# Kernel tuning notes

Measured on AMD Instinct MI355X. Metric: run time of the kernel, lower is better.

The kernel has to match this reference:

```python
import jax, jax.numpy as jnp
import numpy as np

EPS = 1e-10

def setup_inputs() -> dict:
    key = jax.random.key(0)
    k1, k2, k3 = jax.random.split(key, 3)
    B, R, S, C = 4, 4096, 96, 32
    colors = jax.random.uniform(k1, (B, R, S, C), dtype=jnp.float32)
    densities = jax.random.normal(k2, (B, R, S, 1), dtype=jnp.float32)
    # depths: sorted increasing along the sample axis, in a plausible near/far range
    depths = jnp.sort(jax.random.uniform(k3, (B, R, S, 1), dtype=jnp.float32) * 1.8 + 0.8, axis=2)
    return {"colors": colors, "densities": densities, "depths": depths}

def reference(colors, densities, depths):
    # clamp_mode == 'softplus', white_back == False, foreground-only path
    deltas = depths[:, :, 1:] - depths[:, :, :-1]                      # [B,R,S-1,1]
    colors_mid = (colors[:, :, :-1] + colors[:, :, 1:]) * 0.5          # [B,R,S-1,C]
    densities_mid = (densities[:, :, :-1] + densities[:, :, 1:]) * 0.5
    depths_mid = (depths[:, :, :-1] + depths[:, :, 1:]) * 0.5

    densities_mid = jax.nn.softplus(densities_mid - 1.0)
    density_delta = densities_mid * deltas
    alpha = 1.0 - jnp.exp(-density_delta)                              # [B,R,S-1,1]

    ones = jnp.ones_like(alpha[:, :, :1])
    alpha_shifted = jnp.concatenate([ones, 1.0 - alpha + EPS], axis=-2)  # [B,R,S,1]
    transmittance = jnp.cumprod(alpha_shifted, axis=-2)                # per-ray scan
    weights = alpha * transmittance[:, :, :-1]                         # [B,R,S-1,1]
    weight_bg = transmittance[:, :, -1][..., None]                     # [B,R,1,1]

    composite_rgb = jnp.sum(weights * colors_mid, axis=-2)             # [B,R,C]
    weight_total = jnp.sum(weights, axis=2)                            # [B,R,1]
    composite_depth = jnp.sum(weights * depths_mid, axis=-2) / weight_total
    composite_depth = jnp.where(jnp.isnan(composite_depth), jnp.inf, composite_depth)
    composite_depth = jnp.clip(composite_depth, jnp.min(depths), jnp.max(depths))

    composite_rgb = composite_rgb * 2.0 - 1.0
    return composite_rgb, composite_depth, weights, alpha, weight_bg
```

## Files before the change

kernel.cpp:

```cpp
#include <hip/hip_runtime.h>
#include <math.h>

#define NS 96
#define SM1 95
#define NC 32
#define REPS 1e-10f

__global__ __launch_bounds__(128) void raymarch_scan(
    const float* __restrict__ densities,
    const float* __restrict__ depths,
    float* __restrict__ out_depth,
    float* __restrict__ out_w,
    float* __restrict__ out_alpha,
    float* __restrict__ out_wbg,
    float* __restrict__ ws_coeff,
    float* __restrict__ ws_d0,
    float* __restrict__ ws_d1)
{
    const int ray = blockIdx.x;
    const int t = threadIdx.x;

    __shared__ float s_dep[NS];
    __shared__ float s_den[NS];
    __shared__ float s_alpha[SM1];
    __shared__ float s_scan[SM1];
    __shared__ float s_w[SM1];
    __shared__ float s_a[128];
    __shared__ float s_b[128];

    const float* dep = depths + (size_t)ray * NS;
    const float* den = densities + (size_t)ray * NS;

    if (t < NS) {
        s_dep[t] = dep[t];
        s_den[t] = den[t];
    }
    __syncthreads();

    if (t < SM1) {
        float dm = 0.5f * (s_den[t] + s_den[t + 1]) - 1.0f;
        float sp = fmaxf(dm, 0.0f) + log1pf(expf(-fabsf(dm)));
        float dd = sp * (s_dep[t + 1] - s_dep[t]);
        float a = 1.0f - expf(-dd);
        s_alpha[t] = a;
        s_scan[t] = 1.0f - a + REPS;
        out_alpha[(size_t)ray * SM1 + t] = a;
    }
    __syncthreads();

    #pragma unroll
    for (int off = 1; off < SM1; off <<= 1) {
        float x = 1.0f;
        if (t >= off && t < SM1) x = s_scan[t - off];
        __syncthreads();
        if (t >= off && t < SM1) s_scan[t] *= x;
        __syncthreads();
    }

    float w = 0.0f;
    if (t < SM1) {
        float T = (t == 0) ? 1.0f : s_scan[t - 1];
        w = s_alpha[t] * T;
        s_w[t] = w;
        out_w[(size_t)ray * SM1 + t] = w;
    }
    s_a[t] = w;
    s_b[t] = (t < SM1) ? w * 0.5f * (s_dep[t] + s_dep[t + 1]) : 0.0f;
    __syncthreads();

    #pragma unroll
    for (int off = 64; off > 0; off >>= 1) {
        if (t < off) {
            s_a[t] += s_a[t + off];
            s_b[t] += s_b[t + off];
        }
        __syncthreads();
    }

    if (t == 0) {
        out_wbg[ray] = s_scan[SM1 - 1];
        float cd = s_b[0] / s_a[0];
        if (cd != cd) cd = __builtin_inff();
        out_depth[ray] = cd;
        ws_d0[ray] = s_dep[0];
        ws_d1[ray] = s_dep[NS - 1];
    }
    if (t < NS) {
        float wprev = (t >= 1)  ? s_w[t - 1] : 0.0f;
        float wcur  = (t < SM1) ? s_w[t]     : 0.0f;
        ws_coeff[(size_t)ray * NS + t] = 0.5f * (wprev + wcur);
    }
}

__global__ __launch_bounds__(256) void raymarch_color(
    const float* __restrict__ colors,
    const float* __restrict__ ws_coeff,
    float* __restrict__ out_rgb)
{
    const int ray = blockIdx.x;
    const int t = threadIdx.x;

    __shared__ float s_coeff[NS];
    __shared__ float s_red[256 * 4];

    const float4* col4 = (const float4*)(colors + (size_t)ray * NS * NC);
    float4 v0 = col4[t];
    float4 v1 = col4[256 + t];
    float4 v2 = col4[512 + t];

    if (t < NS) s_coeff[t] = ws_coeff[(size_t)ray * NS + t];
    __syncthreads();

    float c0 = s_coeff[t >> 3];
    float c1 = s_coeff[(256 + t) >> 3];
    float c2 = s_coeff[(512 + t) >> 3];
    float4 acc;
    acc.x = fmaf(c0, v0.x, fmaf(c1, v1.x, c2 * v2.x));
    acc.y = fmaf(c0, v0.y, fmaf(c1, v1.y, c2 * v2.y));
    acc.z = fmaf(c0, v0.z, fmaf(c1, v1.z, c2 * v2.z));
    acc.w = fmaf(c0, v0.w, fmaf(c1, v1.w, c2 * v2.w));

    s_red[t * 4 + 0] = acc.x;
    s_red[t * 4 + 1] = acc.y;
    s_red[t * 4 + 2] = acc.z;
    s_red[t * 4 + 3] = acc.w;
    __syncthreads();

    if (t < NC) {
        float sum = 0.0f;
        #pragma unroll
        for (int m = 0; m < 32; ++m) {
            sum += s_red[m * 32 + t];
        }
        out_rgb[(size_t)ray * NC + t] = 2.0f * sum - 1.0f;
    }
}

__global__ __launch_bounds__(256) void raymarch_finalize(
    const float* __restrict__ ws_d0,
    const float* __restrict__ ws_d1,
    float* __restrict__ out_depth,
    int rays)
{
    __shared__ float s_mn[256];
    __shared__ float s_mx[256];
    const int tid = threadIdx.x;

    float mn = __builtin_inff();
    float mx = -__builtin_inff();
    for (int r = tid; r < rays; r += 256) {
        mn = fminf(mn, ws_d0[r]);
        mx = fmaxf(mx, ws_d1[r]);
    }
    s_mn[tid] = mn;
    s_mx[tid] = mx;
    __syncthreads();
    for (int off = 128; off > 0; off >>= 1) {
        if (tid < off) {
            s_mn[tid] = fminf(s_mn[tid], s_mn[tid + off]);
            s_mx[tid] = fmaxf(s_mx[tid], s_mx[tid + off]);
        }
        __syncthreads();
    }
    const float dmin = s_mn[0];
    const float dmax = s_mx[0];

    const int r = blockIdx.x * 256 + tid;
    if (r < rays) {
        float cd = out_depth[r];
        cd = fminf(fmaxf(cd, dmin), dmax);
        out_depth[r] = cd;
    }
}

extern "C" void kernel_launch(void* const* d_in, const int* in_sizes, int n_in,
                              void* d_out, int out_size, void* d_ws, size_t ws_size,
                              hipStream_t stream) {
    const float* colors    = (const float*)d_in[0];
    const float* densities = (const float*)d_in[1];
    const float* depths    = (const float*)d_in[2];

    const int rays = in_sizes[2] / NS;

    float* out = (float*)d_out;
    float* out_rgb   = out;
    float* out_depth = out_rgb + (size_t)rays * NC;
    float* out_w     = out_depth + rays;
    float* out_alpha = out_w + (size_t)rays * SM1;
    float* out_wbg   = out_alpha + (size_t)rays * SM1;

    float* ws       = (float*)d_ws;
    float* ws_d0    = ws;
    float* ws_d1    = ws + rays;
    float* ws_coeff = ws + 2 * (size_t)rays;

    raymarch_scan<<<rays, 128, 0, stream>>>(
        densities, depths,
        out_depth, out_w, out_alpha, out_wbg, ws_coeff, ws_d0, ws_d1);

    raymarch_color<<<rays, 256, 0, stream>>>(colors, ws_coeff, out_rgb);

    raymarch_finalize<<<(rays + 255) / 256, 256, 0, stream>>>(
        ws_d0, ws_d1, out_depth, rays);
}
```

Baseline: 314.7 us.

## Use wavefront-per-ray shuffle scan and multi-ray blocks for color reduction

The scan kernel now maps one 64-lane wavefront to each ray, four rays per block. Each lane handles two samples, and the prefix product and reductions use warp shuffles, which removes shared memory and the many __syncthreads barriers. The color kernel now processes 16 rays per block, with each thread accumulating 48 samples in registers and one xor-shuffle combining the two halves. This replaces the per-ray shared-memory reduction and launches fewer blocks. Fast __expf/__logf intrinsics replace expf/log1pf, which risks small accuracy differences in softplus and alpha. The code also assumes the ray count is divisible by 16.

```diff
diff --git a/kernel.cpp b/kernel.cpp
--- a/kernel.cpp
+++ b/kernel.cpp
@@ -6,7 +6,7 @@
 #define NC 32
 #define REPS 1e-10f
 
-__global__ __launch_bounds__(128) void raymarch_scan(
+__global__ __launch_bounds__(256) void raymarch_scan(
     const float* __restrict__ densities,
     const float* __restrict__ depths,
     float* __restrict__ out_depth,
@@ -17,78 +17,100 @@
     float* __restrict__ ws_d0,
     float* __restrict__ ws_d1)
 {
-    const int ray = blockIdx.x;
-    const int t = threadIdx.x;
-
-    __shared__ float s_dep[NS];
-    __shared__ float s_den[NS];
-    __shared__ float s_alpha[SM1];
-    __shared__ float s_scan[SM1];
-    __shared__ float s_w[SM1];
-    __shared__ float s_a[128];
-    __shared__ float s_b[128];
+    const int ray  = blockIdx.x * 4 + (threadIdx.x >> 6);
+    const int lane = threadIdx.x & 63;
 
     const float* dep = depths + (size_t)ray * NS;
     const float* den = densities + (size_t)ray * NS;
 
-    if (t < NS) {
-        s_dep[t] = dep[t];
-        s_den[t] = den[t];
-    }
-    __syncthreads();
-
-    if (t < SM1) {
-        float dm = 0.5f * (s_den[t] + s_den[t + 1]) - 1.0f;
-        float sp = fmaxf(dm, 0.0f) + log1pf(expf(-fabsf(dm)));
-        float dd = sp * (s_dep[t + 1] - s_dep[t]);
-        float a = 1.0f - expf(-dd);
-        s_alpha[t] = a;
-        s_scan[t] = 1.0f - a + REPS;
-        out_alpha[(size_t)ray * SM1 + t] = a;
-    }
-    __syncthreads();
-
-    #pragma unroll
-    for (int off = 1; off < SM1; off <<= 1) {
-        float x = 1.0f;
-        if (t >= off && t < SM1) x = s_scan[t - off];
-        __syncthreads();
-        if (t >= off && t < SM1) s_scan[t] *= x;
-        __syncthreads();
-    }
-
-    float w = 0.0f;
-    if (t < SM1) {
-        float T = (t == 0) ? 1.0f : s_scan[t - 1];
-        w = s_alpha[t] * T;
-        s_w[t] = w;
-        out_w[(size_t)ray * SM1 + t] = w;
-    }
-    s_a[t] = w;
-    s_b[t] = (t < SM1) ? w * 0.5f * (s_dep[t] + s_dep[t + 1]) : 0.0f;
-    __syncthreads();
-
-    #pragma unroll
-    for (int off = 64; off > 0; off >>= 1) {
-        if (t < off) {
-            s_a[t] += s_a[t + off];
-            s_b[t] += s_b[t + off];
-        }
-        __syncthreads();
-    }
-
-    if (t == 0) {
-        out_wbg[ray] = s_scan[SM1 - 1];
-        float cd = s_b[0] / s_a[0];
+    const int i1 = 64 + lane;
+    float dep0 = dep[lane];
+    float den0 = den[lane];
+    float dep1 = (i1 < NS) ? dep[i1] : 0.0f;
+    float den1 = (i1 < NS) ? den[i1] : 0.0f;
+
+    float dn0 = __shfl(dep0, (lane + 1) & 63);
+    float en0 = __shfl(den0, (lane + 1) & 63);
+    float d64 = __shfl(dep1, 0);
+    float e64 = __shfl(den1, 0);
+    if (lane == 63) { dn0 = d64; en0 = e64; }
+    float dn1 = __shfl(dep1, (lane + 1) & 63);
+    float en1 = __shfl(den1, (lane + 1) & 63);
+
+    float dm0  = 0.5f * (den0 + en0) - 1.0f;
+    float sp0  = fmaxf(dm0, 0.0f) + __logf(1.0f + __expf(-fabsf(dm0)));
+    float a0   = 1.0f - __expf(-sp0 * (dn0 - dep0));
+    float mid0 = 0.5f * (dep0 + dn0);
+
+    float a1 = 0.0f, mid1 = 0.0f;
+    if (lane < 31) {
+        float dm1 = 0.5f * (den1 + en1) - 1.0f;
+        float sp1 = fmaxf(dm1, 0.0f) + __logf(1.0f + __expf(-fabsf(dm1)));
+        a1   = 1.0f - __expf(-sp1 * (dn1 - dep1));
+        mid1 = 0.5f * (dep1 + dn1);
+    }
+
+    float oma0 = 1.0f - a0 + REPS;
+    float oma1 = (lane < 31) ? (1.0f - a1 + REPS) : 1.0f;
+
+    float x = oma0;
+    #pragma unroll
+    for (int off = 1; off < 64; off <<= 1) {
+        float v = __shfl_up(x, off);
+        if (lane >= off) x *= v;
+    }
+    float total0 = __shfl(x, 63);
+
+    float y = oma1;
+    #pragma unroll
+    for (int off = 1; off < 64; off <<= 1) {
+        float v = __shfl_up(y, off);
+        if (lane >= off) y *= v;
+    }
+
+    float xs = __shfl_up(x, 1);
+    float T0 = (lane == 0) ? 1.0f : xs;
+    float w0 = a0 * T0;
+    float ys = __shfl_up(y, 1);
+    float T1 = ((lane == 0) ? 1.0f : ys) * total0;
+    float w1 = a1 * T1;
+
+    float wbg = __shfl(y, 30) * total0;
+
+    float w0p = __shfl_up(w0, 1);
+    float c0  = 0.5f * (((lane == 0) ? 0.0f : w0p) + w0);
+    float w1p = __shfl_up(w1, 1);
+    float w63 = __shfl(w0, 63);
+    float c1  = 0.5f * (((lane == 0) ? w63 : w1p) + w1);
+
+    float wsum = w0 + w1;
+    float dsum = w0 * mid0 + ((lane < 31) ? w1 * mid1 : 0.0f);
+    #pragma unroll
+    for (int off = 32; off > 0; off >>= 1) {
+        wsum += __shfl_xor(wsum, off);
+        dsum += __shfl_xor(dsum, off);
+    }
+
+    const size_t b95 = (size_t)ray * SM1;
+    const size_t b96 = (size_t)ray * NS;
+    out_alpha[b95 + lane] = a0;
+    out_w[b95 + lane]     = w0;
+    ws_coeff[b96 + lane]  = c0;
+    if (lane < 31) {
+        out_alpha[b95 + 64 + lane] = a1;
+        out_w[b95 + 64 + lane]     = w1;
+    }
+    if (lane < 32) {
+        ws_coeff[b96 + 64 + lane] = c1;
+    }
+    float dlast = __shfl(dep1, 31);
+    if (lane == 0) {
+        out_wbg[ray] = wbg;
+        float cd = dsum / wsum;
         if (cd != cd) cd = __builtin_inff();
         out_depth[ray] = cd;
-        ws_d0[ray] = s_dep[0];
-        ws_d1[ray] = s_dep[NS - 1];
-    }
-    if (t < NS) {
-        float wprev = (t >= 1)  ? s_w[t - 1] : 0.0f;
-        float wcur  = (t < SM1) ? s_w[t]     : 0.0f;
-        ws_coeff[(size_t)ray * NS + t] = 0.5f * (wprev + wcur);
+        ws_d0[ray] = dep0;
+        ws_d1[ray] = dlast;
     }
 }
 
@@ -97,42 +119,51 @@
     const float* __restrict__ ws_coeff,
     float* __restrict__ out_rgb)
 {
-    const int ray = blockIdx.x;
-    const int t = threadIdx.x;
-
-    __shared__ float s_coeff[NS];
-    __shared__ float s_red[256 * 4];
+    const int t  = threadIdx.x;
+    const int r0 = blockIdx.x * 16;
+
+    __shared__ float s_coeff[16 * 97];
+
+    #pragma unroll
+    for (int k = 0; k < 6; ++k) {
+        int i = t + k * 256;
+        int r = i / NS, s = i - r * NS;
+        s_coeff[r * 97 + s] = ws_coeff[(size_t)(r0 + r) * NS + s];
+    }
+    __syncthreads();
+
+    const int g = t & 7;
+    const int h = (t >> 3) & 1;
+    const int rl = t >> 4;
+    const int ray = r0 + rl;
+    const int sbase = h * 48;
 
     const float4* col4 = (const float4*)(colors + (size_t)ray * NS * NC);
-    float4 v0 = col4[t];
-    float4 v1 = col4[256 + t];
-    float4 v2 = col4[512 + t];
-
-    if (t < NS) s_coeff[t] = ws_coeff[(size_t)ray * NS + t];
-    __syncthreads();
-
-    float c0 = s_coeff[t >> 3];
-    float c1 = s_coeff[(256 + t) >> 3];
-    float c2 = s_coeff[(512 + t) >> 3];
-    float4 acc;
-    acc.x = fmaf(c0, v0.x, fmaf(c1, v1.x, c2 * v2.x));
-    acc.y = fmaf(c0, v0.y, fmaf(c1, v1.y, c2 * v2.y));
-    acc.z = fmaf(c0, v0.z, fmaf(c1, v1.z, c2 * v2.z));
-    acc.w = fmaf(c0, v0.w, fmaf(c1, v1.w, c2 * v2.w));
-
-    s_red[t * 4 + 0] = acc.x;
-    s_red[t * 4 + 1] = acc.y;
-    s_red[t * 4 + 2] = acc.z;
-    s_red[t * 4 + 3] = acc.w;
-    __syncthreads();
-
-    if (t < NC) {
-        float sum = 0.0f;
-        #pragma unroll
-        for (int m = 0; m < 32; ++m) {
-            sum += s_red[m * 32 + t];
-        }
-        out_rgb[(size_t)ray * NC + t] = 2.0f * sum - 1.0f;
+    const float* cf = &s_coeff[rl * 97 + sbase];
+
+    float4 acc = {0.0f, 0.0f, 0.0f, 0.0f};
+    #pragma unroll 12
+    for (int i = 0; i < 48; ++i) {
+        float4 v = col4[(sbase + i) * 8 + g];
+        float c = cf[i];
+        acc.x = fmaf(c, v.x, acc.x);
+        acc.y = fmaf(c, v.y, acc.y);
+        acc.z = fmaf(c, v.z, acc.z);
+        acc.w = fmaf(c, v.w, acc.w);
+    }
+
+    acc.x += __shfl_xor(acc.x, 8);
+    acc.y += __shfl_xor(acc.y, 8);
+    acc.z += __shfl_xor(acc.z, 8);
+    acc.w += __shfl_xor(acc.w, 8);
+
+    if (h == 0) {
+        float4 o;
+        o.x = 2.0f * acc.x - 1.0f;
+        o.y = 2.0f * acc.y - 1.0f;
+        o.z = 2.0f * acc.z - 1.0f;
+        o.w = 2.0f * acc.w - 1.0f;
+        ((float4*)(out_rgb + (size_t)ray * NC))[g] = o;
     }
 }
 
@@ -194,11 +225,11 @@
     float* ws_d1    = ws + rays;
     float* ws_coeff = ws + 2 * (size_t)rays;
 
-    raymarch_scan<<<rays, 128, 0, stream>>>(
+    raymarch_scan<<<rays / 4, 256, 0, stream>>>(
         densities, depths,
         out_depth, out_w, out_alpha, out_wbg, ws_coeff, ws_d0, ws_d1);
 
-    raymarch_color<<<rays, 256, 0, stream>>>(colors, ws_coeff, out_rgb);
+    raymarch_color<<<rays / 16, 256, 0, stream>>>(colors, ws_coeff, out_rgb);
 
     raymarch_finalize<<<(rays + 255) / 256, 256, 0, stream>>>(
         ws_d0, ws_d1, out_depth, rays);
```

Result: no change. 315.9 us (+0.4%).
